# Kernel tuning notes

Measured on AMD Instinct MI355X. Metric: run time of the kernel, lower is better.

Reference implementation:

```python
import jax, jax.numpy as jnp
import numpy as np

TEMPERATURE = 0.1
POS_WINDOW = 1
NEG_WINDOW = 10


def setup_inputs() -> dict:
    key = jax.random.key(0)
    img_feats = jax.random.normal(key, (8, 2048, 256), dtype=jnp.float32)
    return {"img_feats": img_feats}


def reference(img_feats):
    B, S, D = img_feats.shape
    # L2-normalize along feature dim (matches F.normalize(dim=-1))
    x = img_feats / jnp.clip(jnp.linalg.norm(img_feats, axis=-1, keepdims=True), 1e-12)
    # Full pairwise cosine similarity, scaled by temperature: [B, S, S]
    sim = jnp.einsum('bsd,btd->bst', x, x) / TEMPERATURE

    idx = jnp.arange(S)
    diff = jnp.abs(idx[:, None] - idx[None, :])  # |anchor - other|, [S, S]
    pos_mask = (diff >= 1) & (diff <= POS_WINDOW)   # temporal positives
    neg_mask = diff >= NEG_WINDOW                   # temporal negatives

    # Anchors are valid only if they have >=1 positive and >=1 negative
    pos_count = jnp.sum(pos_mask, axis=1)  # [S]
    valid_t = (pos_count > 0) & (jnp.sum(neg_mask, axis=1) > 0)  # [S]

    E = jnp.exp(sim)  # plain exp, matching the original (no max-subtraction)
    # Per-anchor sum of exp over negatives: [B, S]
    neg_sum = jnp.einsum('bst,st->bs', E, neg_mask.astype(sim.dtype))

    # Per positive pair: -log(exp(sp) / (exp(sp) + neg_sum)) = log(exp(sp)+neg_sum) - sp
    per_pair = jnp.log(E + neg_sum[:, :, None]) - sim  # [B, S, S]
    w = (pos_mask & valid_t[:, None]).astype(sim.dtype)  # [S, S]
    total_loss = jnp.einsum('bst,st->', per_pair, w)

    n_valid = B * jnp.sum(jnp.where(valid_t, pos_count, 0))
    return jnp.where(n_valid > 0, total_loss / n_valid.astype(sim.dtype), 0.0)
```

## Files before the change

### kernel.cpp

```cpp
#include <hip/hip_runtime.h>

#define BATCH 8
#define SEQ   2048
#define DIM   256
#define TINV  10.0f
#define NEGW  10

#define BM 128
#define BN 128
#define BK 64
#define NTILE (SEQ / BM)
#define NPAIR (NTILE * (NTILE + 1) / 2)

typedef float f32x4  __attribute__((ext_vector_type(4)));
typedef short bf16x8 __attribute__((ext_vector_type(8)));

__device__ __forceinline__ unsigned short f2b(float f) {
  union { float f; unsigned u; } v; v.f = f;
  unsigned r = v.u + 0x7fffu + ((v.u >> 16) & 1u);
  return (unsigned short)(r >> 16);
}
__device__ __forceinline__ float b2f(unsigned short u) {
  union { unsigned u; float f; } v; v.u = ((unsigned)u) << 16;
  return v.f;
}

__global__ void normalize_bf16_kernel(const float* __restrict__ x,
                                      unsigned short* __restrict__ xb,
                                      float* __restrict__ zero_region) {
  if (blockIdx.x < 64) {
    zero_region[blockIdx.x * 256 + threadIdx.x] = 0.f;
  } else if (blockIdx.x == 64 && threadIdx.x < 16) {
    zero_region[16384 + threadIdx.x] = 0.f;
  }
  int row  = blockIdx.x * 4 + (threadIdx.x >> 6);
  int lane = threadIdx.x & 63;
  const float4 v = reinterpret_cast<const float4*>(x + (size_t)row * DIM)[lane];
  float ss = v.x * v.x + v.y * v.y + v.z * v.z + v.w * v.w;
#pragma unroll
  for (int off = 32; off; off >>= 1) ss += __shfl_xor(ss, off, 64);
  float rn = 1.0f / fmaxf(sqrtf(ss), 1e-12f);
  ushort4 o;
  o.x = f2b(v.x * rn); o.y = f2b(v.y * rn);
  o.z = f2b(v.z * rn); o.w = f2b(v.w * rn);
  reinterpret_cast<ushort4*>(xb + (size_t)row * DIM)[lane] = o;
}

__global__ __launch_bounds__(256, 2)
void sim_negsum_kernel(const unsigned short* __restrict__ xb,
                       float* __restrict__ negsum) {
  const int b = blockIdx.y;
  int ti = 0, rem = blockIdx.x;
  while (rem >= NTILE - ti) { rem -= NTILE - ti; ti++; }
  const int tj = ti + rem;
  const bool diag = (ti == tj);
  const int s0 = ti * BM, t0 = tj * BN;

  __shared__ unsigned short Asm[BM * BK];
  __shared__ unsigned short Bsm[BN * BK];

  const unsigned short* Ag = xb + (size_t)b * SEQ * DIM + (size_t)s0 * DIM;
  const unsigned short* Bg = xb + (size_t)b * SEQ * DIM + (size_t)t0 * DIM;

  const int tid  = threadIdx.x;
  const int wid  = tid >> 6;
  const int lane = tid & 63;
  const int wm   = wid >> 1;
  const int wn   = wid & 1;
  const int kg   = lane >> 4;
  const int cl   = lane & 15;

  f32x4 acc[4][4];
#pragma unroll
  for (int m = 0; m < 4; ++m)
#pragma unroll
    for (int n = 0; n < 4; ++n)
      acc[m][n] = (f32x4){0.f, 0.f, 0.f, 0.f};

  for (int kt = 0; kt < DIM / BK; ++kt) {
#pragma unroll
    for (int i = 0; i < 4; ++i) {
      int c = i * 256 + tid;
      int row = c >> 3, slot = c & 7;
      const size_t goff = (size_t)row * DIM + kt * BK + slot * 8;
      uint4 va = *reinterpret_cast<const uint4*>(Ag + goff);
      uint4 vb = *reinterpret_cast<const uint4*>(Bg + goff);
      int loff = row * 128 + ((slot ^ (row & 7)) << 4);
      *reinterpret_cast<uint4*>(reinterpret_cast<char*>(Asm) + loff) = va;
      *reinterpret_cast<uint4*>(reinterpret_cast<char*>(Bsm) + loff) = vb;
    }
    __syncthreads();

#pragma unroll
    for (int kk = 0; kk < BK / 32; ++kk) {
      bf16x8 af[4], bfr[4];
#pragma unroll
      for (int m = 0; m < 4; ++m) {
        int r = wm * 64 + m * 16 + cl;
        int slot = kk * 4 + kg;
        af[m] = *reinterpret_cast<const bf16x8*>(
            reinterpret_cast<const char*>(Asm) + r * 128 + ((slot ^ (r & 7)) << 4));
      }
#pragma unroll
      for (int n = 0; n < 4; ++n) {
        int r = wn * 64 + n * 16 + cl;
        int slot = kk * 4 + kg;
        bfr[n] = *reinterpret_cast<const bf16x8*>(
            reinterpret_cast<const char*>(Bsm) + r * 128 + ((slot ^ (r & 7)) << 4));
      }
#pragma unroll
      for (int m = 0; m < 4; ++m)
#pragma unroll
        for (int n = 0; n < 4; ++n)
          acc[m][n] = __builtin_amdgcn_mfma_f32_16x16x32_bf16(
              af[m], bfr[n], acc[m][n], 0, 0, 0);
    }
    __syncthreads();
  }

  float rowpart[4][4];
  float colpart[4];
#pragma unroll
  for (int m = 0; m < 4; ++m)
#pragma unroll
    for (int r = 0; r < 4; ++r) rowpart[m][r] = 0.f;
#pragma unroll
  for (int n = 0; n < 4; ++n) colpart[n] = 0.f;

#pragma unroll
  for (int m = 0; m < 4; ++m) {
#pragma unroll
    for (int n = 0; n < 4; ++n) {
#pragma unroll
      for (int r = 0; r < 4; ++r) {
        int srow = s0 + wm * 64 + m * 16 + (kg << 2) + r;
        int tcol = t0 + wn * 64 + n * 16 + cl;
        int d = srow - tcol; d = d < 0 ? -d : d;
        float e = (d >= NEGW) ? __expf(acc[m][n][r] * TINV) : 0.f;
        rowpart[m][r] += e;
        colpart[n]    += e;
      }
    }
  }

#pragma unroll
  for (int off = 1; off <= 8; off <<= 1)
#pragma unroll
    for (int m = 0; m < 4; ++m)
#pragma unroll
      for (int r = 0; r < 4; ++r)
        rowpart[m][r] += __shfl_xor(rowpart[m][r], off, 64);
  if (cl == 0) {
#pragma unroll
    for (int m = 0; m < 4; ++m)
#pragma unroll
      for (int r = 0; r < 4; ++r)
        atomicAdd(&negsum[(size_t)b * SEQ + s0 + wm * 64 + m * 16 + (kg << 2) + r],
                  rowpart[m][r]);
  }

  if (!diag) {
#pragma unroll
    for (int off = 16; off <= 32; off <<= 1)
#pragma unroll
      for (int n = 0; n < 4; ++n)
        colpart[n] += __shfl_xor(colpart[n], off, 64);
    if (lane < 16) {
#pragma unroll
      for (int n = 0; n < 4; ++n)
        atomicAdd(&negsum[(size_t)b * SEQ + t0 + wn * 64 + n * 16 + lane],
                  colpart[n]);
    }
  }
}

#define POS_BLOCKS 256
#define POS_WAVES  (POS_BLOCKS * 4)

__device__ __forceinline__ int negcnt(int s) {
  int a = s - (NEGW - 1);      if (a < 0) a = 0;
  int b = SEQ - NEGW - s;      if (b < 0) b = 0;
  return a + b;
}

__global__ __launch_bounds__(256)
void pos_loss_kernel(const unsigned short* __restrict__ xb,
                     const float* __restrict__ negsum,
                     float* __restrict__ loss) {
  __shared__ float red[4];
  const int wid  = threadIdx.x >> 6;
  const int lane = threadIdx.x & 63;
  const int gw   = blockIdx.x * 4 + wid;
  const int NP   = BATCH * (SEQ - 1);

  float term = 0.f;
  for (int p = gw; p < NP; p += POS_WAVES) {
    int b = p / (SEQ - 1), s = p % (SEQ - 1);
    const ushort4 u = reinterpret_cast<const ushort4*>(
        xb + ((size_t)b * SEQ + s) * DIM)[lane];
    const ushort4 w = reinterpret_cast<const ushort4*>(
        xb + ((size_t)b * SEQ + s + 1) * DIM)[lane];
    float dot = b2f(u.x) * b2f(w.x) + b2f(u.y) * b2f(w.y) +
                b2f(u.z) * b2f(w.z) + b2f(u.w) * b2f(w.w);
#pragma unroll
    for (int off = 32; off; off >>= 1) dot += __shfl_xor(dot, off, 64);
    float sp = dot * TINV;
    float e  = __expf(sp);
    if (lane == 0 && negcnt(s) > 0)
      term += logf(e + negsum[(size_t)b * SEQ + s]) - sp;
    if (lane == 1 && negcnt(s + 1) > 0)
      term += logf(e + negsum[(size_t)b * SEQ + s + 1]) - sp;
  }
#pragma unroll
  for (int off = 32; off; off >>= 1) term += __shfl_xor(term, off, 64);
  if (lane == 0) red[wid] = term;
  __syncthreads();
  if (threadIdx.x == 0)
    atomicAdd(loss, red[0] + red[1] + red[2] + red[3]);
}

__global__ void finalize_kernel(const float* __restrict__ loss,
                                float* __restrict__ out) {
  int lane = threadIdx.x;
  int cnt = 0;
  for (int s = lane; s < SEQ; s += 64) {
    if (negcnt(s) > 0) cnt += (s > 0) + (s < SEQ - 1);
  }
#pragma unroll
  for (int off = 32; off; off >>= 1) cnt += __shfl_xor(cnt, off, 64);
  if (lane == 0) {
    long long nv = (long long)BATCH * cnt;
    out[0] = (nv > 0) ? loss[0] / (float)nv : 0.0f;
  }
}

extern "C" void kernel_launch(void* const* d_in, const int* in_sizes, int n_in,
                              void* d_out, int out_size, void* d_ws, size_t ws_size,
                              hipStream_t stream) {
  const float* x = (const float*)d_in[0];
  unsigned short* xb = (unsigned short*)d_ws;
  const size_t XB_BYTES = (size_t)BATCH * SEQ * DIM * 2;
  const size_t NS_BYTES = (size_t)BATCH * SEQ * 4;
  float* negsum = (float*)((char*)d_ws + XB_BYTES);
  float* loss   = (float*)((char*)d_ws + XB_BYTES + NS_BYTES);

  normalize_bf16_kernel<<<(BATCH * SEQ) / 4, 256, 0, stream>>>(x, xb, negsum);

  dim3 g2(NPAIR, BATCH);
  sim_negsum_kernel<<<g2, 256, 0, stream>>>(xb, negsum);

  pos_loss_kernel<<<POS_BLOCKS, 256, 0, stream>>>(xb, negsum, loss);

  finalize_kernel<<<1, 64, 0, stream>>>(loss, (float*)d_out);
}
```

Measured before the change: 57.83 us.

## Double-buffer GEMM tiles via direct global-to-LDS loads and reuse positive-pair similarities

```diff
diff --git a/kernel.cpp b/kernel.cpp
--- a/kernel.cpp
+++ b/kernel.cpp
@@ -46,9 +46,21 @@
   reinterpret_cast<ushort4*>(xb + (size_t)row * DIM)[lane] = o;
 }
 
+__device__ __forceinline__ void stage8(const unsigned short* __restrict__ G,
+                                       unsigned short* dst_wave_uniform,
+                                       int rowbase, int rl, int p, int kt) {
+  int row = rowbase + rl;
+  const unsigned short* src =
+      G + (size_t)row * DIM + kt * BK + ((p ^ (row & 7)) << 3);
+  __builtin_amdgcn_global_load_lds(
+      (const __attribute__((address_space(1))) void*)src,
+      (__attribute__((address_space(3))) void*)dst_wave_uniform, 16, 0, 0);
+}
+
 __global__ __launch_bounds__(256, 2)
 void sim_negsum_kernel(const unsigned short* __restrict__ xb,
-                       float* __restrict__ negsum) {
+                       float* __restrict__ negsum,
+                       float* __restrict__ sp_out) {
   const int b = blockIdx.y;
   int ti = 0, rem = blockIdx.x;
   while (rem >= NTILE - ti) { rem -= NTILE - ti; ti++; }
@@ -56,8 +68,8 @@
   const bool diag = (ti == tj);
   const int s0 = ti * BM, t0 = tj * BN;
 
-  __shared__ unsigned short Asm[BM * BK];
-  __shared__ unsigned short Bsm[BN * BK];
+  __shared__ unsigned short Asm[2][BM * BK];
+  __shared__ unsigned short Bsm[2][BM * BK];
 
   const unsigned short* Ag = xb + (size_t)b * SEQ * DIM + (size_t)s0 * DIM;
   const unsigned short* Bg = xb + (size_t)b * SEQ * DIM + (size_t)t0 * DIM;
@@ -69,6 +81,8 @@
   const int wn   = wid & 1;
   const int kg   = lane >> 4;
   const int cl   = lane & 15;
+  const int rl   = lane >> 3;
+  const int p    = lane & 7;
 
   f32x4 acc[4][4];
 #pragma unroll
@@ -77,19 +91,29 @@
     for (int n = 0; n < 4; ++n)
       acc[m][n] = (f32x4){0.f, 0.f, 0.f, 0.f};
 
+#define STAGE_KT(buf, kt)                                                     \
+  do {                                                                        \
+    _Pragma("unroll")                                                         \
+    for (int it = 0; it < 4; ++it) {                                          \
+      int rowbase = wid * 32 + it * 8;                                        \
+      stage8(Ag, &Asm[buf][rowbase * BK], rowbase, rl, p, kt);                \
+      if (!diag) stage8(Bg, &Bsm[buf][rowbase * BK], rowbase, rl, p, kt);     \
+    }                                                                         \
+  } while (0)
+
+  const unsigned short* Bsm0 = diag ? &Asm[0][0] : &Bsm[0][0];
+  const unsigned short* Bsm1 = diag ? &Asm[1][0] : &Bsm[1][0];
+
+  STAGE_KT(0, 0);
+  __syncthreads();
+
+#pragma unroll
   for (int kt = 0; kt < DIM / BK; ++kt) {
-#pragma unroll
-    for (int i = 0; i < 4; ++i) {
-      int c = i * 256 + tid;
-      int row = c >> 3, slot = c & 7;
-      const size_t goff = (size_t)row * DIM + kt * BK + slot * 8;
-      uint4 va = *reinterpret_cast<const uint4*>(Ag + goff);
-      uint4 vb = *reinterpret_cast<const uint4*>(Bg + goff);
-      int loff = row * 128 + ((slot ^ (row & 7)) << 4);
-      *reinterpret_cast<uint4*>(reinterpret_cast<char*>(Asm) + loff) = va;
-      *reinterpret_cast<uint4*>(reinterpret_cast<char*>(Bsm) + loff) = vb;
-    }
-    __syncthreads();
+    if (kt < 3) {
+      if (kt & 1) STAGE_KT(0, kt + 1); else STAGE_KT(1, kt + 1);
+    }
+    const unsigned short* Acur = &Asm[kt & 1][0];
+    const unsigned short* Bcur = (kt & 1) ? Bsm1 : Bsm0;
 
 #pragma unroll
     for (int kk = 0; kk < BK / 32; ++kk) {
@@ -99,14 +123,14 @@
         int r = wm * 64 + m * 16 + cl;
         int slot = kk * 4 + kg;
         af[m] = *reinterpret_cast<const bf16x8*>(
-            reinterpret_cast<const char*>(Asm) + r * 128 + ((slot ^ (r & 7)) << 4));
+            reinterpret_cast<const char*>(Acur) + r * 128 + ((slot ^ (r & 7)) << 4));
       }
 #pragma unroll
       for (int n = 0; n < 4; ++n) {
         int r = wn * 64 + n * 16 + cl;
         int slot = kk * 4 + kg;
         bfr[n] = *reinterpret_cast<const bf16x8*>(
-            reinterpret_cast<const char*>(Bsm) + r * 128 + ((slot ^ (r & 7)) << 4));
+            reinterpret_cast<const char*>(Bcur) + r * 128 + ((slot ^ (r & 7)) << 4));
       }
 #pragma unroll
       for (int m = 0; m < 4; ++m)
@@ -117,6 +141,7 @@
     }
     __syncthreads();
   }
+#undef STAGE_KT
 
   float rowpart[4][4];
   float colpart[4];
@@ -135,10 +160,13 @@
       for (int r = 0; r < 4; ++r) {
         int srow = s0 + wm * 64 + m * 16 + (kg << 2) + r;
         int tcol = t0 + wn * 64 + n * 16 + cl;
-        int d = srow - tcol; d = d < 0 ? -d : d;
+        int diff = tcol - srow;
+        int d = diff < 0 ? -diff : diff;
         float e = (d >= NEGW) ? __expf(acc[m][n][r] * TINV) : 0.f;
         rowpart[m][r] += e;
         colpart[n]    += e;
+        if (diff == 1)
+          sp_out[(size_t)b * (SEQ - 1) + srow] = acc[m][n][r] * TINV;
       }
     }
   }
@@ -173,9 +201,6 @@
     }
   }
 }
-
-#define POS_BLOCKS 256
-#define POS_WAVES  (POS_BLOCKS * 4)
 
 __device__ __forceinline__ int negcnt(int s) {
   int a = s - (NEGW - 1);      if (a < 0) a = 0;
@@ -184,36 +209,23 @@
 }
 
 __global__ __launch_bounds__(256)
-void pos_loss_kernel(const unsigned short* __restrict__ xb,
+void pos_loss_kernel(const float* __restrict__ sp,
                      const float* __restrict__ negsum,
                      float* __restrict__ loss) {
   __shared__ float red[4];
-  const int wid  = threadIdx.x >> 6;
-  const int lane = threadIdx.x & 63;
-  const int gw   = blockIdx.x * 4 + wid;
-  const int NP   = BATCH * (SEQ - 1);
-
+  const int NP = BATCH * (SEQ - 1);
+  int pidx = blockIdx.x * 256 + threadIdx.x;
   float term = 0.f;
-  for (int p = gw; p < NP; p += POS_WAVES) {
-    int b = p / (SEQ - 1), s = p % (SEQ - 1);
-    const ushort4 u = reinterpret_cast<const ushort4*>(
-        xb + ((size_t)b * SEQ + s) * DIM)[lane];
-    const ushort4 w = reinterpret_cast<const ushort4*>(
-        xb + ((size_t)b * SEQ + s + 1) * DIM)[lane];
-    float dot = b2f(u.x) * b2f(w.x) + b2f(u.y) * b2f(w.y) +
-                b2f(u.z) * b2f(w.z) + b2f(u.w) * b2f(w.w);
-#pragma unroll
-    for (int off = 32; off; off >>= 1) dot += __shfl_xor(dot, off, 64);
-    float sp = dot * TINV;
-    float e  = __expf(sp);
-    if (lane == 0 && negcnt(s) > 0)
-      term += logf(e + negsum[(size_t)b * SEQ + s]) - sp;
-    if (lane == 1 && negcnt(s + 1) > 0)
-      term += logf(e + negsum[(size_t)b * SEQ + s + 1]) - sp;
+  if (pidx < NP) {
+    int b = pidx / (SEQ - 1), s = pidx % (SEQ - 1);
+    float spv = sp[pidx];
+    float e = __expf(spv);
+    if (negcnt(s) > 0)     term += logf(e + negsum[(size_t)b * SEQ + s])     - spv;
+    if (negcnt(s + 1) > 0) term += logf(e + negsum[(size_t)b * SEQ + s + 1]) - spv;
   }
 #pragma unroll
   for (int off = 32; off; off >>= 1) term += __shfl_xor(term, off, 64);
-  if (lane == 0) red[wid] = term;
+  if ((threadIdx.x & 63) == 0) red[threadIdx.x >> 6] = term;
   __syncthreads();
   if (threadIdx.x == 0)
     atomicAdd(loss, red[0] + red[1] + red[2] + red[3]);
@@ -243,13 +255,15 @@
   const size_t NS_BYTES = (size_t)BATCH * SEQ * 4;
   float* negsum = (float*)((char*)d_ws + XB_BYTES);
   float* loss   = (float*)((char*)d_ws + XB_BYTES + NS_BYTES);
+  float* sp     = (float*)((char*)d_ws + XB_BYTES + NS_BYTES + 64);
 
   normalize_bf16_kernel<<<(BATCH * SEQ) / 4, 256, 0, stream>>>(x, xb, negsum);
 
   dim3 g2(NPAIR, BATCH);
-  sim_negsum_kernel<<<g2, 256, 0, stream>>>(xb, negsum);
-
-  pos_loss_kernel<<<POS_BLOCKS, 256, 0, stream>>>(xb, negsum, loss);
+  sim_negsum_kernel<<<g2, 256, 0, stream>>>(xb, negsum, sp);
+
+  const int NP = BATCH * (SEQ - 1);
+  pos_loss_kernel<<<(NP + 255) / 256, 256, 0, stream>>>(sp, negsum, loss);
 
   finalize_kernel<<<1, 64, 0, stream>>>(loss, (float*)d_out);
 }
```

New measurement: 47.07 us. 18.6% less time.
